# Kernel optimization log

Measured on AMD Instinct MI355X. Metric: run time of the kernel, lower is better.

The kernel has to match this reference:

```python
import jax, jax.numpy as jnp
import numpy as np

E = 128          # number of bot groups (envs)
NB = 256         # bots per group
DQ = DK = DV = 256
D = DQ + DK + DV # 768
COM_RANGE = 15.0
KV_NOISE = 0.05
NEG = -1000000.0


def setup_inputs() -> dict:
    key = jax.random.key(0)
    k1, k2, k3, k4 = jax.random.split(key, 4)
    N = E * NB
    qkv = jax.random.normal(k1, (N, D), dtype=jnp.float32)
    # audibility mask: [N_total, n_per_group]; mask[bot_slice] -> [n, n] per group
    mask = jax.random.bernoulli(k2, 0.9, (N, NB))
    # 2D positions in a 30x30 arena so ~half of pairs fall within com_range
    bot_pos = jax.random.uniform(k3, (N, 2), dtype=jnp.float32, minval=0.0, maxval=30.0)
    # kv noise: zero on the q part [:K_DIM], gaussian(std=kv_noise) on k,v part
    noise = jnp.concatenate(
        [jnp.zeros((N, DQ), jnp.float32),
         KV_NOISE * jax.random.normal(k4, (N, DK + DV), dtype=jnp.float32)],
        axis=-1)
    s = jnp.float32(0.0)  # nn.Parameter init
    return {"qkv": qkv, "mask": mask, "bot_pos": bot_pos, "noise": noise, "s": s}


def reference(qkv, mask, bot_pos, noise, s):
    # noise injection on k,v channels (noise is zero on q channels)
    qkv = qkv + noise
    scale_s = jnp.abs(s) + 1.0

    # all bot groups are equal-sized -> batch the per-slice loop as [E, NB, ...]
    qkv_g = qkv.reshape(E, NB, D)
    q = qkv_g[..., :DQ] * scale_s
    k = qkv_g[..., DQ:DQ + DK]
    v = qkv_g[..., DQ + DK:]

    # pairwise-distance range mask per group
    pos = bot_pos.reshape(E, NB, 2)
    bdiff = pos[:, None, :, :] - pos[:, :, None, :]          # [E, NB, NB, 2]
    range_mask = jnp.linalg.norm(bdiff, axis=-1) < COM_RANGE  # [E, NB, NB]

    audible = mask.reshape(E, NB, NB) & range_mask            # [E, NB, NB]

    # SDPA with additive mask (torch adds -1e6 where masked)
    scores = jnp.einsum('eqd,ekd->eqk', q, k) / jnp.sqrt(jnp.float32(DK))
    scores = scores + jnp.where(audible, 0.0, NEG)
    attn = jax.nn.softmax(scores, axis=-1)
    x = jnp.einsum('eqk,ekd->eqd', attn, v)                   # [E, NB, DV]

    # zero out bots that hear nobody
    x = x * audible.any(axis=-1, keepdims=True)
    return x.reshape(E * NB, DV)
```

## Files before the change

### kernel.cpp

```cpp
#include <hip/hip_runtime.h>
#include <hip/hip_bf16.h>
#include <stdint.h>


#define EE   128
#define NBB  256
#define DDIM 768
#define NEGV (-1000000.0f)

typedef __attribute__((ext_vector_type(8))) short short8;
typedef __attribute__((ext_vector_type(4))) float f32x4;

__device__ __forceinline__ unsigned short f2bf(float f){
  union { float f; unsigned u; } v; v.f = f;
  return (unsigned short)((v.u + 0x7FFFu + ((v.u >> 16) & 1u)) >> 16);
}
__device__ __forceinline__ unsigned short cvt1(float f){
  __hip_bfloat16 h = __float2bfloat16(f);
  unsigned short u; __builtin_memcpy(&u, &h, 2); return u;
}

__device__ __forceinline__ void gload16(const void* g, void* l){
  __builtin_amdgcn_global_load_lds((const __attribute__((address_space(1))) unsigned*)g,
                                   (__attribute__((address_space(3))) unsigned*)l, 16, 0, 0);
}

__global__ void k_prep_vt(const float* __restrict__ qkv, const float* __restrict__ noise,
                          unsigned short* __restrict__ Vt){
  __shared__ unsigned short tile[64 * 66];
  const int b = blockIdx.x;
  const int e = b >> 4, t4 = b & 15;
  const int k0 = (t4 >> 2) << 6, d0 = (t4 & 3) << 6;
  const int u = threadIdx.x & 15, r = threadIdx.x >> 4;
  #pragma unroll
  for(int i = 0; i < 4; ++i){
    const int kl = r + (i << 4);
    const size_t off = ((size_t)(e*NBB + k0 + kl)) * DDIM + 512 + d0 + (u << 2);
    f32x4 v  = *(const f32x4*)(qkv   + off);
    f32x4 nz = *(const f32x4*)(noise + off);
    const int base = kl * 66 + (u << 2);
    tile[base+0] = f2bf(v[0]+nz[0]); tile[base+1] = f2bf(v[1]+nz[1]);
    tile[base+2] = f2bf(v[2]+nz[2]); tile[base+3] = f2bf(v[3]+nz[3]);
  }
  __syncthreads();
  #pragma unroll
  for(int i = 0; i < 4; ++i){
    const int dl = r + (i << 4);
    unsigned short o0 = tile[(u*4+0)*66 + dl];
    unsigned short o1 = tile[(u*4+1)*66 + dl];
    unsigned short o2 = tile[(u*4+2)*66 + dl];
    unsigned short o3 = tile[(u*4+3)*66 + dl];
    *(ushort4*)(Vt + ((size_t)(e*NBB + d0 + dl)) * NBB + k0 + (u << 2)) =
        make_ushort4(o0, o1, o2, o3);
  }
}

__launch_bounds__(256, 2)
__global__ void k_attn(const float* __restrict__ qkv, const float* __restrict__ noise,
                       const float* __restrict__ sp,
                       const unsigned char* __restrict__ m8, const int* __restrict__ m32,
                       const float* __restrict__ pos,
                       const unsigned short* __restrict__ Vt,
                       float* __restrict__ out){
  extern __shared__ unsigned char smem[];
  unsigned short* ldsKV = (unsigned short*)smem;
  unsigned short* ldsP  = (unsigned short*)(smem + 32768);
  unsigned*       audL  = (unsigned*)(smem + 65536);
  float*          posx  = (float*)(smem + 67584);
  float*          posy  = (float*)(smem + 68608);

  const int bid = blockIdx.x;
  const int e   = ((bid & 7) << 4) + (bid >> 5);
  const int qq  = (bid >> 3) & 3;
  const int tid  = threadIdx.x;
  const int wave = tid >> 6;
  const int lane = tid & 63;
  const int g    = lane >> 4;
  const int u    = lane & 15;
  const int q0   = qq * 64 + wave * 16;
  const size_t ebase = (size_t)e * NBB;

  {
    const float2 p = *(const float2*)(pos + (ebase + tid) * 2);
    posx[tid] = p.x; posy[tid] = p.y;
  }
  const unsigned probe = ((const unsigned*)m32)[tid & 63];
  const int isInt = !__any(probe > 1u);
  __syncthreads();
  #pragma unroll
  for(int h = 0; h < 2; ++h){
    const int w   = tid + h * 256;
    const int row = w >> 3;
    const int j   = w & 7;
    const float qx = posx[qq*64 + row], qy = posy[qq*64 + row];
    const size_t mbase = (ebase + qq*64 + row) * NBB + j * 32;
    unsigned wd = 0u;
    if(isInt){
      #pragma unroll
      for(int i = 0; i < 8; ++i){
        const int4 mv = *(const int4*)(m32 + mbase + i * 4);
        const int mvals[4] = {mv.x, mv.y, mv.z, mv.w};
        #pragma unroll
        for(int jj = 0; jj < 4; ++jj){
          const int kk = i * 4 + jj;
          const int k  = j * 32 + kk;
          const float dx = posx[k] - qx, dy = posy[k] - qy;
          const float d2 = __fadd_rn(__fmul_rn(dx, dx), __fmul_rn(dy, dy));
          if((mvals[jj] != 0) && (sqrtf(d2) < 15.0f)) wd |= 1u << kk;
        }
      }
    } else {
      #pragma unroll
      for(int i = 0; i < 2; ++i){
        const int4 mv = *(const int4*)(m8 + mbase + i * 16);
        const int mvals[4] = {mv.x, mv.y, mv.z, mv.w};
        #pragma unroll
        for(int jj = 0; jj < 4; ++jj)
          #pragma unroll
          for(int b = 0; b < 4; ++b){
            const int kk = i * 16 + jj * 4 + b;
            const int k  = j * 32 + kk;
            const float dx = posx[k] - qx, dy = posy[k] - qy;
            const float d2 = __fadd_rn(__fmul_rn(dx, dx), __fmul_rn(dy, dy));
            if((((unsigned)mvals[jj] >> (8 * b)) & 0xFFu) && (sqrtf(d2) < 15.0f)) wd |= 1u << kk;
          }
      }
    }
    audL[w] = wd;
  }

  const float scale = fabsf(sp[0]) + 1.0f;
  short8 qf[8];
  {
    const float* qrow = qkv + (ebase + q0 + u) * DDIM;
    #pragma unroll
    for(int dk = 0; dk < 8; ++dk){
      f32x4 a = *(const f32x4*)(qrow + dk*32 + g*8);
      f32x4 b = *(const f32x4*)(qrow + dk*32 + g*8 + 4);
      short8 f;
      f[0]=cvt1(a[0]*scale); f[1]=cvt1(a[1]*scale); f[2]=cvt1(a[2]*scale); f[3]=cvt1(a[3]*scale);
      f[4]=cvt1(b[0]*scale); f[5]=cvt1(b[1]*scale); f[6]=cvt1(b[2]*scale); f[7]=cvt1(b[3]*scale);
      qf[dk] = f;
    }
  }

  const f32x4 zero4 = {0.f, 0.f, 0.f, 0.f};
  f32x4 acc[16];
  #pragma unroll
  for(int nt = 0; nt < 16; ++nt) acc[nt] = zero4;

  #pragma unroll
  for(int kq = 0; kq < 4; ++kq){
    __syncthreads();
    {
      #pragma unroll
      for(int i = 0; i < 16; ++i){
        const int row = wave*16 + i;
        const size_t goff = (ebase + kq*64 + row) * DDIM + 256 + lane*4;
        f32x4 a  = *(const f32x4*)(qkv + goff);
        f32x4 nz = *(const f32x4*)(noise + goff);
        uint2 o;
        o.x = (unsigned)cvt1(a[0]+nz[0]) | ((unsigned)cvt1(a[1]+nz[1]) << 16);
        o.y = (unsigned)cvt1(a[2]+nz[2]) | ((unsigned)cvt1(a[3]+nz[3]) << 16);
        const int col = (lane*4) ^ ((row & 7) << 3);
        *(uint2*)(ldsKV + row*256 + col) = o;
      }
    }
    __syncthreads();
    #pragma unroll
    for(int nth = 0; nth < 4; ++nth){
      const unsigned short* kr = ldsKV + (nth*16 + u) * 256;
      const int sw = (u & 7) << 3;
      #pragma unroll
      for(int dk = 0; dk < 8; ++dk){
        short8 kb = *(const short8*)(kr + ((dk*32 + g*8) ^ sw));
        acc[kq*4 + nth] = __builtin_amdgcn_mfma_f32_16x16x32_bf16(qf[dk], kb, acc[kq*4 + nth], 0, 0, 0);
      }
    }
  }

  __syncthreads();
  {
    const unsigned short* base = Vt + (ebase + 0) * 256;
    #pragma unroll
    for(int i = 0; i < 8; ++i){
      const int lrow = wave*16 + i*2 + (lane >> 5);
      const int col  = ((lane & 31) * 8) ^ ((lrow & 7) << 3);
      gload16(base + (size_t)lrow * 256 + col, ldsKV + (wave*16 + i*2) * 256);
    }
  }

  unsigned anybits = 0u;
  unsigned short* Pw = ldsP + wave * 4096;
  #pragma unroll
  for(int r = 0; r < 4; ++r){
    const int qw = g*4 + r;
    unsigned w[8];
    #pragma unroll
    for(int j = 0; j < 8; ++j) w[j] = audL[(wave*16 + qw)*8 + j];
    const unsigned anyw = w[0]|w[1]|w[2]|w[3]|w[4]|w[5]|w[6]|w[7];
    anybits |= (anyw ? 1u : 0u) << r;
    float m = -3.0e38f;
    #pragma unroll
    for(int nt = 0; nt < 16; ++nt){
      const unsigned bit = (w[nt >> 1] >> (((nt & 1) << 4) + u)) & 1u;
      float s = acc[nt][r] * 0.0625f + (bit ? 0.0f : NEGV);
      acc[nt][r] = s;
      m = fmaxf(m, s);
    }
    #pragma unroll
    for(int d = 1; d < 16; d <<= 1) m = fmaxf(m, __shfl_xor(m, d));
    float ssum = 0.0f;
    #pragma unroll
    for(int nt = 0; nt < 16; ++nt){
      const float p = __expf(acc[nt][r] - m);
      acc[nt][r] = p;
      ssum += p;
    }
    #pragma unroll
    for(int d = 1; d < 16; d <<= 1) ssum += __shfl_xor(ssum, d);
    const float inv = 1.0f / ssum;
    const int swp = (qw & 7) << 3;
    #pragma unroll
    for(int nt = 0; nt < 16; ++nt)
      Pw[qw*256 + ((nt*16 + u) ^ swp)] = f2bf(acc[nt][r] * inv);
  }

  short8 pa[8];
  {
    const unsigned short* pr = Pw + u*256;
    const int swp = (u & 7) << 3;
    #pragma unroll
    for(int kt = 0; kt < 8; ++kt)
      pa[kt] = *(const short8*)(pr + ((kt*32 + g*8) ^ swp));
  }

  __syncthreads();
  #pragma unroll
  for(int dqt = 0; dqt < 4; ++dqt){
    f32x4 xacc[4];
    #pragma unroll
    for(int dt = 0; dt < 4; ++dt) xacc[dt] = zero4;
    #pragma unroll
    for(int dt = 0; dt < 4; ++dt){
      const unsigned short* vr = ldsKV + (dt*16 + u) * 256;
      const int sw = (u & 7) << 3;
      #pragma unroll
      for(int kt = 0; kt < 8; ++kt){
        short8 bv = *(const short8*)(vr + ((kt*32 + g*8) ^ sw));
        xacc[dt] = __builtin_amdgcn_mfma_f32_16x16x32_bf16(pa[kt], bv, xacc[dt], 0, 0, 0);
      }
    }
    #pragma unroll
    for(int r = 0; r < 4; ++r){
      const float zf = ((anybits >> r) & 1u) ? 1.0f : 0.0f;
      float* orow = out + (ebase + q0 + g*4 + r) * 256 + dqt*64;
      #pragma unroll
      for(int dt = 0; dt < 4; ++dt)
        orow[dt*16 + u] = xacc[dt][r] * zf;
    }
    if(dqt < 3){
      __syncthreads();
      const unsigned short* base = Vt + (ebase + (size_t)(dqt+1) * 64) * 256;
      #pragma unroll
      for(int i = 0; i < 8; ++i){
        const int lrow = wave*16 + i*2 + (lane >> 5);
        const int col  = ((lane & 31) * 8) ^ ((lrow & 7) << 3);
        gload16(base + (size_t)lrow * 256 + col, ldsKV + (wave*16 + i*2) * 256);
      }
      __syncthreads();
    }
  }
}

extern "C" void kernel_launch(void* const* d_in, const int* in_sizes, int n_in,
                              void* d_out, int out_size, void* d_ws, size_t ws_size,
                              hipStream_t stream){
  (void)in_sizes; (void)n_in; (void)out_size; (void)ws_size;
  const float* qkv   = (const float*)d_in[0];
  const void*  mask  = d_in[1];
  const float* pos   = (const float*)d_in[2];
  const float* noise = (const float*)d_in[3];
  const float* sp    = (const float*)d_in[4];

  unsigned short* Vt = (unsigned short*)d_ws;
  float* outp = (float*)d_out;

  k_prep_vt<<<2048, 256, 0, stream>>>(qkv, noise, Vt);

  hipFuncSetAttribute((const void*)k_attn, hipFuncAttributeMaxDynamicSharedMemorySize, 69632);
  k_attn<<<512, 256, 69632, stream>>>(qkv, noise, sp,
                                      (const unsigned char*)mask, (const int*)mask,
                                      pos, Vt, outp);
}
```

Baseline: 66.90 us.

## Keep softmax probabilities in registers via transposed QK MFMA and permlane swaps

The QK^T MFMA operands are swapped so each lane holds a column of scores for one query row. Softmax then reduces within the lane and across lane groups. The probabilities are converted to bf16 and rearranged into the PV A-operand layout with permlane32/16 swaps, which removes the LDS staging buffer for P. This halves the shared memory footprint, so launch bounds rise to 4 blocks per CU for higher occupancy, at the cost of register pressure and possible spills.

```diff
diff --git a/kernel.cpp b/kernel.cpp
--- a/kernel.cpp
+++ b/kernel.cpp
@@ -18,6 +18,32 @@
 __device__ __forceinline__ unsigned short cvt1(float f){
   __hip_bfloat16 h = __float2bfloat16(f);
   unsigned short u; __builtin_memcpy(&u, &h, 2); return u;
+}
+__device__ __forceinline__ unsigned pk2(float lo, float hi){
+  return (unsigned)cvt1(lo) | ((unsigned)cvt1(hi) << 16);
+}
+
+__device__ __forceinline__ void swap32(unsigned &a, unsigned &b){
+#if __has_builtin(__builtin_amdgcn_permlane32_swap)
+  auto r = __builtin_amdgcn_permlane32_swap(a, b, false, false);
+  a = r[0]; b = r[1];
+#else
+  const int up = threadIdx.x & 32;
+  const unsigned ax = __shfl_xor(a, 32), bx = __shfl_xor(b, 32);
+  const unsigned na = up ? bx : a, nb = up ? b : ax;
+  a = na; b = nb;
+#endif
+}
+__device__ __forceinline__ void swap16(unsigned &a, unsigned &b){
+#if __has_builtin(__builtin_amdgcn_permlane16_swap)
+  auto r = __builtin_amdgcn_permlane16_swap(a, b, false, false);
+  a = r[0]; b = r[1];
+#else
+  const int odd = threadIdx.x & 16;
+  const unsigned ax = __shfl_xor(a, 16), bx = __shfl_xor(b, 16);
+  const unsigned na = odd ? bx : a, nb = odd ? b : ax;
+  a = na; b = nb;
+#endif
 }
 
 __device__ __forceinline__ void gload16(const void* g, void* l){
@@ -55,7 +81,7 @@
   }
 }
 
-__launch_bounds__(256, 2)
+__launch_bounds__(256, 4)
 __global__ void k_attn(const float* __restrict__ qkv, const float* __restrict__ noise,
                        const float* __restrict__ sp,
                        const unsigned char* __restrict__ m8, const int* __restrict__ m32,
@@ -64,10 +90,9 @@
                        float* __restrict__ out){
   extern __shared__ unsigned char smem[];
   unsigned short* ldsKV = (unsigned short*)smem;
-  unsigned short* ldsP  = (unsigned short*)(smem + 32768);
-  unsigned*       audL  = (unsigned*)(smem + 65536);
-  float*          posx  = (float*)(smem + 67584);
-  float*          posy  = (float*)(smem + 68608);
+  unsigned*       audL  = (unsigned*)(smem + 32768);
+  float*          posx  = (float*)(smem + 34816);
+  float*          posy  = (float*)(smem + 35840);
 
   const int bid = blockIdx.x;
   const int e   = ((bid & 7) << 4) + (bid >> 5);
@@ -160,8 +185,8 @@
         f32x4 a  = *(const f32x4*)(qkv + goff);
         f32x4 nz = *(const f32x4*)(noise + goff);
         uint2 o;
-        o.x = (unsigned)cvt1(a[0]+nz[0]) | ((unsigned)cvt1(a[1]+nz[1]) << 16);
-        o.y = (unsigned)cvt1(a[2]+nz[2]) | ((unsigned)cvt1(a[3]+nz[3]) << 16);
+        o.x = pk2(a[0]+nz[0], a[1]+nz[1]);
+        o.y = pk2(a[2]+nz[2], a[3]+nz[3]);
         const int col = (lane*4) ^ ((row & 7) << 3);
         *(uint2*)(ldsKV + row*256 + col) = o;
       }
@@ -174,7 +199,7 @@
       #pragma unroll
       for(int dk = 0; dk < 8; ++dk){
         short8 kb = *(const short8*)(kr + ((dk*32 + g*8) ^ sw));
-        acc[kq*4 + nth] = __builtin_amdgcn_mfma_f32_16x16x32_bf16(qf[dk], kb, acc[kq*4 + nth], 0, 0, 0);
+        acc[kq*4 + nth] = __builtin_amdgcn_mfma_f32_16x16x32_bf16(kb, qf[dk], acc[kq*4 + nth], 0, 0, 0);
       }
     }
   }
@@ -190,49 +215,57 @@
     }
   }
 
-  unsigned anybits = 0u;
-  unsigned short* Pw = ldsP + wave * 4096;
-  #pragma unroll
-  for(int r = 0; r < 4; ++r){
-    const int qw = g*4 + r;
-    unsigned w[8];
-    #pragma unroll
-    for(int j = 0; j < 8; ++j) w[j] = audL[(wave*16 + qw)*8 + j];
-    const unsigned anyw = w[0]|w[1]|w[2]|w[3]|w[4]|w[5]|w[6]|w[7];
-    anybits |= (anyw ? 1u : 0u) << r;
-    float m = -3.0e38f;
-    #pragma unroll
-    for(int nt = 0; nt < 16; ++nt){
-      const unsigned bit = (w[nt >> 1] >> (((nt & 1) << 4) + u)) & 1u;
-      float s = acc[nt][r] * 0.0625f + (bit ? 0.0f : NEGV);
-      acc[nt][r] = s;
-      m = fmaxf(m, s);
-    }
-    #pragma unroll
-    for(int d = 1; d < 16; d <<= 1) m = fmaxf(m, __shfl_xor(m, d));
-    float ssum = 0.0f;
-    #pragma unroll
-    for(int nt = 0; nt < 16; ++nt){
-      const float p = __expf(acc[nt][r] - m);
-      acc[nt][r] = p;
-      ssum += p;
-    }
-    #pragma unroll
-    for(int d = 1; d < 16; d <<= 1) ssum += __shfl_xor(ssum, d);
-    const float inv = 1.0f / ssum;
-    const int swp = (qw & 7) << 3;
-    #pragma unroll
-    for(int nt = 0; nt < 16; ++nt)
-      Pw[qw*256 + ((nt*16 + u) ^ swp)] = f2bf(acc[nt][r] * inv);
-  }
+  unsigned wmask[8];
+  {
+    const unsigned* arow = audL + (wave*16 + u) * 8;
+    #pragma unroll
+    for(int j = 0; j < 8; ++j) wmask[j] = arow[j];
+  }
+  const unsigned anyw = wmask[0]|wmask[1]|wmask[2]|wmask[3]|wmask[4]|wmask[5]|wmask[6]|wmask[7];
+  const unsigned long long rowsAny = __ballot(anyw != 0u);
+
+  float m0=-3.0e38f, m1=-3.0e38f, m2=-3.0e38f, m3=-3.0e38f;
+  #pragma unroll
+  for(int nt = 0; nt < 16; ++nt){
+    const unsigned wv = wmask[nt >> 1] >> (((nt & 1) << 4) + g*4);
+    f32x4 s = acc[nt];
+    s[0] = s[0]*0.0625f + ((wv      & 1u) ? 0.0f : NEGV);
+    s[1] = s[1]*0.0625f + (((wv>>1) & 1u) ? 0.0f : NEGV);
+    s[2] = s[2]*0.0625f + (((wv>>2) & 1u) ? 0.0f : NEGV);
+    s[3] = s[3]*0.0625f + (((wv>>3) & 1u) ? 0.0f : NEGV);
+    acc[nt] = s;
+    m0 = fmaxf(m0, s[0]); m1 = fmaxf(m1, s[1]);
+    m2 = fmaxf(m2, s[2]); m3 = fmaxf(m3, s[3]);
+  }
+  float mx = fmaxf(fmaxf(m0, m1), fmaxf(m2, m3));
+  mx = fmaxf(mx, __shfl_xor(mx, 16));
+  mx = fmaxf(mx, __shfl_xor(mx, 32));
+  float s0=0.f, s1=0.f, s2=0.f, s3=0.f;
+  #pragma unroll
+  for(int nt = 0; nt < 16; ++nt){
+    f32x4 p = acc[nt];
+    p[0] = __expf(p[0] - mx); p[1] = __expf(p[1] - mx);
+    p[2] = __expf(p[2] - mx); p[3] = __expf(p[3] - mx);
+    acc[nt] = p;
+    s0 += p[0]; s1 += p[1]; s2 += p[2]; s3 += p[3];
+  }
+  float ssum = (s0 + s1) + (s2 + s3);
+  ssum += __shfl_xor(ssum, 16);
+  ssum += __shfl_xor(ssum, 32);
+  const float inv = 1.0f / ssum;
 
   short8 pa[8];
-  {
-    const unsigned short* pr = Pw + u*256;
-    const int swp = (u & 7) << 3;
-    #pragma unroll
-    for(int kt = 0; kt < 8; ++kt)
-      pa[kt] = *(const short8*)(pr + ((kt*32 + g*8) ^ swp));
+  #pragma unroll
+  for(int kt = 0; kt < 8; ++kt){
+    unsigned cE = pk2(acc[2*kt][0]*inv,   acc[2*kt][1]*inv);
+    unsigned dE = pk2(acc[2*kt][2]*inv,   acc[2*kt][3]*inv);
+    unsigned cO = pk2(acc[2*kt+1][0]*inv, acc[2*kt+1][1]*inv);
+    unsigned dO = pk2(acc[2*kt+1][2]*inv, acc[2*kt+1][3]*inv);
+    swap32(cE, cO); swap16(cE, cO);
+    swap32(dE, dO); swap16(dE, dO);
+    union { short8 s; unsigned w[4]; } pk;
+    pk.w[0] = cE; pk.w[1] = dE; pk.w[2] = cO; pk.w[3] = dO;
+    pa[kt] = pk.s;
   }
 
   __syncthreads();
@@ -253,7 +286,7 @@
     }
     #pragma unroll
     for(int r = 0; r < 4; ++r){
-      const float zf = ((anybits >> r) & 1u) ? 1.0f : 0.0f;
+      const float zf = ((rowsAny >> (g*4 + r)) & 1ull) ? 1.0f : 0.0f;
       float* orow = out + (ebase + q0 + g*4 + r) * 256 + dqt*64;
       #pragma unroll
       for(int dt = 0; dt < 4; ++dt)
@@ -288,8 +321,8 @@
 
   k_prep_vt<<<2048, 256, 0, stream>>>(qkv, noise, Vt);
 
-  hipFuncSetAttribute((const void*)k_attn, hipFuncAttributeMaxDynamicSharedMemorySize, 69632);
-  k_attn<<<512, 256, 69632, stream>>>(qkv, noise, sp,
+  hipFuncSetAttribute((const void*)k_attn, hipFuncAttributeMaxDynamicSharedMemorySize, 36864);
+  k_attn<<<512, 256, 36864, stream>>>(qkv, noise, sp,
                                       (const unsigned char*)mask, (const int*)mask,
                                       pos, Vt, outp);
 }
```

Result: slower. 106.8 us (+59.7%).
